# Kernel tuning notes

Measured on AMD Instinct MI355X. Metric: run time of the kernel, lower is better.

The kernel has to match this reference:

```python
import jax, jax.numpy as jnp
import numpy as np


def setup_inputs() -> dict:
    key = jax.random.key(0)
    ks = jax.random.split(key, 5)
    B, C, H, W = 8, 256, 64, 64
    Cr = 32  # in_channels // reduction_ratio
    s_in = 1.0 / np.sqrt(C)
    x = jax.random.normal(ks[0], (B, C, H, W), dtype=jnp.float32)
    Wq = jax.random.normal(ks[1], (Cr, C), dtype=jnp.float32) * s_in
    Wk = jax.random.normal(ks[2], (Cr, C), dtype=jnp.float32) * s_in
    Wv = jax.random.normal(ks[3], (C, C), dtype=jnp.float32) * s_in
    bq = jnp.zeros((Cr,), dtype=jnp.float32)
    bk = jnp.zeros((Cr,), dtype=jnp.float32)
    bv = jnp.zeros((C,), dtype=jnp.float32)
    gamma = jnp.ones((1,), dtype=jnp.float32)
    return {"x": x, "Wq": Wq, "bq": bq, "Wk": Wk, "bk": bk, "Wv": Wv, "bv": bv, "gamma": gamma}


def reference(x, Wq, bq, Wk, bk, Wv, bv, gamma):
    B, C, H, W = x.shape
    N = H * W
    xf = x.reshape(B, C, N)  # 1x1 conv == per-pixel linear over channels
    q = jnp.einsum('oc,bcn->bon', Wq, xf) + bq[None, :, None]   # [B, Cr, N]
    k = jnp.einsum('oc,bcn->bon', Wk, xf) + bk[None, :, None]   # [B, Cr, N]
    v = jnp.einsum('oc,bcn->bon', Wv, xf) + bv[None, :, None]   # [B, C, N]
    # correlations[b, i, j] = sum_c q[b, c, i] * k[b, c, j]
    corr = jnp.einsum('bci,bcj->bij', q, k)                     # [B, N, N]
    # NOTE: softmax over dim=1 (the i / query axis), as in the original torch code
    beta = jax.nn.softmax(corr, axis=1)
    att = gamma[0] * jnp.einsum('bci,bij->bcj', v, beta)        # [B, C, N]
    return att.reshape(B, C, H, W) + x
```

## Files before the change

### kernel.cpp

```cpp
#include <hip/hip_runtime.h>
#include <hip/hip_bf16.h>

typedef short bf16x8 __attribute__((ext_vector_type(8)));
typedef float f32x4 __attribute__((ext_vector_type(4)));
typedef unsigned short u16;

#define LOG2E 1.44269504088896340736f

__device__ __forceinline__ u16 f2bf(float f) {
    unsigned u = __float_as_uint(f);
    u += 0x7fffu + ((u >> 16) & 1u);
    return (u16)(u >> 16);
}
__device__ __forceinline__ float bf2f(u16 h) {
    return __uint_as_float(((unsigned)h) << 16);
}

__global__ void k_prep(const float* __restrict__ Wq, const float* __restrict__ bq,
                       const float* __restrict__ Wk, const float* __restrict__ bk,
                       const float* __restrict__ Wv, const float* __restrict__ bv,
                       u16* __restrict__ Whi, u16* __restrict__ Wlo,
                       float* __restrict__ bias) {
    int idx = blockIdx.x * 256 + threadIdx.x;
    if (idx >= 320 * 256) return;
    int row = idx >> 8, c = idx & 255;
    float w, b;
    if (row < 256)      { w = Wv[row * 256 + c];                  b = bv[row]; }
    else if (row < 288) { w = Wq[(row - 256) * 256 + c] * LOG2E;  b = bq[row - 256] * LOG2E; }
    else                { w = Wk[(row - 288) * 256 + c];          b = bk[row - 288]; }
    u16 hi = f2bf(w);
    Whi[idx] = hi;
    Wlo[idx] = f2bf(w - bf2f(hi));
    if (c == 0) bias[row] = b;
}

#define XPAD 264

__global__ __launch_bounds__(256) void k_proj(
    const float* __restrict__ x, const u16* __restrict__ Whi,
    const u16* __restrict__ Wlo, const float* __restrict__ bias,
    u16* __restrict__ qt, u16* __restrict__ kt, u16* __restrict__ vbf) {
    __shared__ __attribute__((aligned(16))) u16 xh[64 * XPAD];
    __shared__ __attribute__((aligned(16))) u16 xl[64 * XPAD];
    int bid = blockIdx.x;
    int b = bid & 7, nt = bid >> 3;
    int n0 = nt * 64;
    int t = threadIdx.x;
    int lane = t & 63, w = t >> 6;
    int lr = lane & 15, lk = lane >> 4;

    {
        int n = t & 63;
        int cg = t >> 6;
        for (int it = 0; it < 8; ++it) {
            int c8 = (it * 4 + cg) * 8;
            bf16x8 hv, lv;
#pragma unroll
            for (int u = 0; u < 8; ++u) {
                float xv = x[((size_t)(b * 256 + c8 + u)) * 4096 + n0 + n];
                u16 hu = f2bf(xv);
                hv[u] = (short)hu;
                lv[u] = (short)f2bf(xv - bf2f(hu));
            }
            *(bf16x8*)&xh[n * XPAD + c8] = hv;
            *(bf16x8*)&xl[n * XPAD + c8] = lv;
        }
    }
    __syncthreads();

    f32x4 acc[5][4];
#pragma unroll
    for (int i = 0; i < 5; i++)
#pragma unroll
        for (int j = 0; j < 4; j++) acc[i][j] = (f32x4){0.f, 0.f, 0.f, 0.f};

    for (int cs = 0; cs < 8; ++cs) {
        int c0 = cs * 32;
        bf16x8 ah[5], al[5], bh[4], bl[4];
#pragma unroll
        for (int mt = 0; mt < 5; ++mt) {
            int row = (w * 5 + mt) * 16 + lr;
            ah[mt] = *(const bf16x8*)&Whi[row * 256 + c0 + lk * 8];
            al[mt] = *(const bf16x8*)&Wlo[row * 256 + c0 + lk * 8];
        }
#pragma unroll
        for (int ns = 0; ns < 4; ++ns) {
            int np = ns * 16 + lr;
            bh[ns] = *(const bf16x8*)&xh[np * XPAD + c0 + lk * 8];
            bl[ns] = *(const bf16x8*)&xl[np * XPAD + c0 + lk * 8];
        }
#pragma unroll
        for (int mt = 0; mt < 5; ++mt)
#pragma unroll
            for (int ns = 0; ns < 4; ++ns) {
                acc[mt][ns] = __builtin_amdgcn_mfma_f32_16x16x32_bf16(ah[mt], bh[ns], acc[mt][ns], 0, 0, 0);
                acc[mt][ns] = __builtin_amdgcn_mfma_f32_16x16x32_bf16(ah[mt], bl[ns], acc[mt][ns], 0, 0, 0);
                acc[mt][ns] = __builtin_amdgcn_mfma_f32_16x16x32_bf16(al[mt], bh[ns], acc[mt][ns], 0, 0, 0);
            }
    }

#pragma unroll
    for (int mt = 0; mt < 5; ++mt) {
        int tile = w * 5 + mt;
#pragma unroll
        for (int ns = 0; ns < 4; ++ns) {
#pragma unroll
            for (int r = 0; r < 4; ++r) {
                int row = tile * 16 + lk * 4 + r;
                int n = n0 + ns * 16 + lr;
                float val = acc[mt][ns][r] + bias[row];
                if (row < 256) {
                    vbf[((size_t)(b * 256 + row)) * 4096 + n] = f2bf(val);
                } else if (row < 288) {
                    u16 hi = f2bf(val);
                    size_t base = ((size_t)(b * 4096 + n)) * 64 + (row - 256);
                    qt[base] = hi;
                    qt[base + 32] = f2bf(val - bf2f(hi));
                } else {
                    u16 hi = f2bf(val);
                    size_t base = ((size_t)(b * 4096 + n)) * 64 + (row - 288);
                    kt[base] = hi;
                    kt[base + 32] = f2bf(val - bf2f(hi));
                }
            }
        }
    }
}

#define PSTR 72

__global__ __launch_bounds__(256, 2) void k_attn(
    const u16* __restrict__ qt, const u16* __restrict__ kt,
    const u16* __restrict__ vbf, const float* __restrict__ x,
    const float* __restrict__ gamma, float* __restrict__ out) {
    __shared__ __attribute__((aligned(16))) u16 P[2][4][16][PSTR];
    __shared__ float sc[2][64];
    __shared__ float lbuf[64];
    int bid = blockIdx.x;
    int b = bid & 7, jt = bid >> 3;
    int t = threadIdx.x;
    int lane = t & 63, w = t >> 6;
    int lr = lane & 15, lk = lane >> 4;
    int j0 = jt * 64;
    int jw = j0 + w * 16;

    size_t kb = ((size_t)(b * 4096 + jw + lr)) * 64 + lk * 8;
    bf16x8 khi = *(const bf16x8*)&kt[kb];
    bf16x8 klo = *(const bf16x8*)&kt[kb + 32];

    f32x4 acc[4][4];
#pragma unroll
    for (int i = 0; i < 4; i++)
#pragma unroll
        for (int j = 0; j < 4; j++) acc[i][j] = (f32x4){0.f, 0.f, 0.f, 0.f};
    float mcur = -3.0e38f, lsum = 0.f;
    const f32x4 zero = {0.f, 0.f, 0.f, 0.f};

    for (int it = 0; it < 64; ++it) {
        int i0 = it * 64;
        int p = it & 1;

        bf16x8 qh[4], ql[4];
#pragma unroll
        for (int g = 0; g < 4; ++g) {
            size_t qb = ((size_t)(b * 4096 + i0 + g * 16 + lr)) * 64 + lk * 8;
            qh[g] = *(const bf16x8*)&qt[qb];
            ql[g] = *(const bf16x8*)&qt[qb + 32];
        }
        bf16x8 av[2][4];
#pragma unroll
        for (int ks = 0; ks < 2; ++ks)
#pragma unroll
            for (int ct = 0; ct < 4; ++ct)
                av[ks][ct] = *(const bf16x8*)&vbf[((size_t)(b * 256 + w * 64 + ct * 16 + lr)) * 4096
                                                  + i0 + ks * 32 + lk * 8];

        f32x4 s[4];
#pragma unroll
        for (int g = 0; g < 4; ++g) {
            s[g] = __builtin_amdgcn_mfma_f32_16x16x32_bf16(qh[g], khi, zero, 0, 0, 0);
            s[g] = __builtin_amdgcn_mfma_f32_16x16x32_bf16(qh[g], klo, s[g], 0, 0, 0);
            s[g] = __builtin_amdgcn_mfma_f32_16x16x32_bf16(ql[g], khi, s[g], 0, 0, 0);
        }

        float tm = -3.0e38f;
#pragma unroll
        for (int g = 0; g < 4; ++g)
            tm = fmaxf(tm, fmaxf(fmaxf(s[g][0], s[g][1]), fmaxf(s[g][2], s[g][3])));
        tm = fmaxf(tm, __shfl_xor(tm, 16));
        tm = fmaxf(tm, __shfl_xor(tm, 32));
        float mnew = fmaxf(mcur, tm);
        float scale = exp2f(mcur - mnew);
        mcur = mnew;
        lsum *= scale;
#pragma unroll
        for (int g = 0; g < 4; ++g) {
            float p0 = exp2f(s[g][0] - mcur), p1 = exp2f(s[g][1] - mcur);
            float p2 = exp2f(s[g][2] - mcur), p3 = exp2f(s[g][3] - mcur);
            lsum += (p0 + p1) + (p2 + p3);
            uint2 pk;
            pk.x = ((unsigned)f2bf(p1) << 16) | f2bf(p0);
            pk.y = ((unsigned)f2bf(p3) << 16) | f2bf(p2);
            *(uint2*)&P[p][w][lr][g * 16 + lk * 4] = pk;
        }
        if (lk == 0) sc[p][w * 16 + lr] = scale;
        __syncthreads();

        float rs[4];
#pragma unroll
        for (int js = 0; js < 4; ++js) rs[js] = sc[p][js * 16 + lr];
        if (__any((rs[0] != 1.f) | (rs[1] != 1.f) | (rs[2] != 1.f) | (rs[3] != 1.f))) {
#pragma unroll
            for (int ct = 0; ct < 4; ++ct)
#pragma unroll
                for (int js = 0; js < 4; ++js)
#pragma unroll
                    for (int r = 0; r < 4; ++r) acc[ct][js][r] *= rs[js];
        }
#pragma unroll
        for (int ks = 0; ks < 2; ++ks) {
            bf16x8 bp[4];
#pragma unroll
            for (int js = 0; js < 4; ++js)
                bp[js] = *(const bf16x8*)&P[p][js][lr][ks * 32 + lk * 8];
#pragma unroll
            for (int ct = 0; ct < 4; ++ct)
#pragma unroll
                for (int js = 0; js < 4; ++js)
                    acc[ct][js] = __builtin_amdgcn_mfma_f32_16x16x32_bf16(av[ks][ct], bp[js], acc[ct][js], 0, 0, 0);
        }
    }

    lsum += __shfl_xor(lsum, 16);
    lsum += __shfl_xor(lsum, 32);
    __syncthreads();
    if (lk == 0) lbuf[w * 16 + lr] = lsum;
    __syncthreads();
    float g = gamma[0];
    float linv[4];
#pragma unroll
    for (int js = 0; js < 4; ++js) linv[js] = g / lbuf[js * 16 + lr];
#pragma unroll
    for (int ct = 0; ct < 4; ++ct)
#pragma unroll
        for (int r = 0; r < 4; ++r) {
            int c = w * 64 + ct * 16 + lk * 4 + r;
            size_t base = ((size_t)(b * 256 + c)) * 4096 + j0;
#pragma unroll
            for (int js = 0; js < 4; ++js) {
                int j = js * 16 + lr;
                out[base + j] = acc[ct][js][r] * linv[js] + x[base + j];
            }
        }
}

extern "C" void kernel_launch(void* const* d_in, const int* in_sizes, int n_in,
                              void* d_out, int out_size, void* d_ws, size_t ws_size,
                              hipStream_t stream) {
    const float* x = (const float*)d_in[0];
    const float* Wq = (const float*)d_in[1];
    const float* bq = (const float*)d_in[2];
    const float* Wk = (const float*)d_in[3];
    const float* bk = (const float*)d_in[4];
    const float* Wv = (const float*)d_in[5];
    const float* bv = (const float*)d_in[6];
    const float* gamma = (const float*)d_in[7];

    char* ws = (char*)d_ws;
    u16* Whi = (u16*)ws;
    u16* Wlo = (u16*)(ws + 163840);
    float* bias = (float*)(ws + 327680);
    u16* qt = (u16*)(ws + 329216);
    u16* kt = (u16*)(ws + 329216 + 4194304);
    u16* vbf = (u16*)(ws + 329216 + 8388608);

    k_prep<<<320, 256, 0, stream>>>(Wq, bq, Wk, bk, Wv, bv, Whi, Wlo, bias);
    k_proj<<<512, 256, 0, stream>>>(x, Whi, Wlo, bias, qt, kt, vbf);
    k_attn<<<512, 256, 0, stream>>>(qt, kt, vbf, x, gamma, (float*)d_out);
}
```

Before: 356.3 us.

## Split attention block into producer and consumer waves for softmax/PV overlap

Each block now has 8 waves instead of 4. Four producer waves compute QK scores and the online-softmax tile for the next step into the double-buffered LDS P and scale arrays. Four consumer waves load V and run the PV MFMAs on the current tile, with one barrier per iteration. The aim is to overlap the exp and softmax work with the matrix accumulation and to spread V-load latency across more waves. The cost is doubled thread count per block, idle producers at the epilogue, and different occupancy and register limits from the new launch bounds.

```diff
diff --git a/kernel.cpp b/kernel.cpp
--- a/kernel.cpp
+++ b/kernel.cpp
@@ -129,7 +129,7 @@
 
 #define PSTR 72
 
-__global__ __launch_bounds__(256, 2) void k_attn(
+__global__ __launch_bounds__(512, 4) void k_attn(
     const u16* __restrict__ qt, const u16* __restrict__ kt,
     const u16* __restrict__ vbf, const float* __restrict__ x,
     const float* __restrict__ gamma, float* __restrict__ out) {
@@ -142,24 +142,23 @@
     int lane = t & 63, w = t >> 6;
     int lr = lane & 15, lk = lane >> 4;
     int j0 = jt * 64;
-    int jw = j0 + w * 16;
-
-    size_t kb = ((size_t)(b * 4096 + jw + lr)) * 64 + lk * 8;
+    int wp = w & 3;
+    bool is_prod = (w < 4);
+
+    size_t kb = ((size_t)(b * 4096 + j0 + wp * 16 + lr)) * 64 + lk * 8;
     bf16x8 khi = *(const bf16x8*)&kt[kb];
     bf16x8 klo = *(const bf16x8*)&kt[kb + 32];
 
+    float mcur = -3.0e38f, lsum = 0.f;
     f32x4 acc[4][4];
 #pragma unroll
     for (int i = 0; i < 4; i++)
 #pragma unroll
         for (int j = 0; j < 4; j++) acc[i][j] = (f32x4){0.f, 0.f, 0.f, 0.f};
-    float mcur = -3.0e38f, lsum = 0.f;
     const f32x4 zero = {0.f, 0.f, 0.f, 0.f};
 
-    for (int it = 0; it < 64; ++it) {
-        int i0 = it * 64;
-        int p = it & 1;
-
+    auto prod_step = [&](int it) {
+        int i0 = it * 64, p = it & 1;
         bf16x8 qh[4], ql[4];
 #pragma unroll
         for (int g = 0; g < 4; ++g) {
@@ -167,14 +166,6 @@
             qh[g] = *(const bf16x8*)&qt[qb];
             ql[g] = *(const bf16x8*)&qt[qb + 32];
         }
-        bf16x8 av[2][4];
-#pragma unroll
-        for (int ks = 0; ks < 2; ++ks)
-#pragma unroll
-            for (int ct = 0; ct < 4; ++ct)
-                av[ks][ct] = *(const bf16x8*)&vbf[((size_t)(b * 256 + w * 64 + ct * 16 + lr)) * 4096
-                                                  + i0 + ks * 32 + lk * 8];
-
         f32x4 s[4];
 #pragma unroll
         for (int g = 0; g < 4; ++g) {
@@ -182,7 +173,6 @@
             s[g] = __builtin_amdgcn_mfma_f32_16x16x32_bf16(qh[g], klo, s[g], 0, 0, 0);
             s[g] = __builtin_amdgcn_mfma_f32_16x16x32_bf16(ql[g], khi, s[g], 0, 0, 0);
         }
-
         float tm = -3.0e38f;
 #pragma unroll
         for (int g = 0; g < 4; ++g)
@@ -201,11 +191,18 @@
             uint2 pk;
             pk.x = ((unsigned)f2bf(p1) << 16) | f2bf(p0);
             pk.y = ((unsigned)f2bf(p3) << 16) | f2bf(p2);
-            *(uint2*)&P[p][w][lr][g * 16 + lk * 4] = pk;
-        }
-        if (lk == 0) sc[p][w * 16 + lr] = scale;
-        __syncthreads();
-
+            *(uint2*)&P[p][wp][lr][g * 16 + lk * 4] = pk;
+        }
+        if (lk == 0) sc[p][wp * 16 + lr] = scale;
+    };
+
+    auto cons_step = [&](int it) {
+        int i0 = it * 64, p = it & 1;
+        bf16x8 av0[4];
+#pragma unroll
+        for (int ct = 0; ct < 4; ++ct)
+            av0[ct] = *(const bf16x8*)&vbf[((size_t)(b * 256 + wp * 64 + ct * 16 + lr)) * 4096
+                                           + i0 + lk * 8];
         float rs[4];
 #pragma unroll
         for (int js = 0; js < 4; ++js) rs[js] = sc[p][js * 16 + lr];
@@ -217,41 +214,69 @@
 #pragma unroll
                     for (int r = 0; r < 4; ++r) acc[ct][js][r] *= rs[js];
         }
-#pragma unroll
-        for (int ks = 0; ks < 2; ++ks) {
+        bf16x8 av1[4];
+#pragma unroll
+        for (int ct = 0; ct < 4; ++ct)
+            av1[ct] = *(const bf16x8*)&vbf[((size_t)(b * 256 + wp * 64 + ct * 16 + lr)) * 4096
+                                           + i0 + 32 + lk * 8];
+        {
             bf16x8 bp[4];
 #pragma unroll
             for (int js = 0; js < 4; ++js)
-                bp[js] = *(const bf16x8*)&P[p][js][lr][ks * 32 + lk * 8];
+                bp[js] = *(const bf16x8*)&P[p][js][lr][lk * 8];
 #pragma unroll
             for (int ct = 0; ct < 4; ++ct)
 #pragma unroll
                 for (int js = 0; js < 4; ++js)
-                    acc[ct][js] = __builtin_amdgcn_mfma_f32_16x16x32_bf16(av[ks][ct], bp[js], acc[ct][js], 0, 0, 0);
-        }
-    }
-
-    lsum += __shfl_xor(lsum, 16);
-    lsum += __shfl_xor(lsum, 32);
+                    acc[ct][js] = __builtin_amdgcn_mfma_f32_16x16x32_bf16(av0[ct], bp[js], acc[ct][js], 0, 0, 0);
+        }
+        {
+            bf16x8 bp[4];
+#pragma unroll
+            for (int js = 0; js < 4; ++js)
+                bp[js] = *(const bf16x8*)&P[p][js][lr][32 + lk * 8];
+#pragma unroll
+            for (int ct = 0; ct < 4; ++ct)
+#pragma unroll
+                for (int js = 0; js < 4; ++js)
+                    acc[ct][js] = __builtin_amdgcn_mfma_f32_16x16x32_bf16(av1[ct], bp[js], acc[ct][js], 0, 0, 0);
+        }
+    };
+
+    if (is_prod) prod_step(0);
+    for (int tt = 0; tt < 64; ++tt) {
+        __syncthreads();
+        if (is_prod) {
+            if (tt < 63) prod_step(tt + 1);
+        } else {
+            cons_step(tt);
+        }
+    }
+
+    if (is_prod) {
+        lsum += __shfl_xor(lsum, 16);
+        lsum += __shfl_xor(lsum, 32);
+        if (lk == 0) lbuf[wp * 16 + lr] = lsum;
+    }
     __syncthreads();
-    if (lk == 0) lbuf[w * 16 + lr] = lsum;
-    __syncthreads();
-    float g = gamma[0];
-    float linv[4];
-#pragma unroll
-    for (int js = 0; js < 4; ++js) linv[js] = g / lbuf[js * 16 + lr];
-#pragma unroll
-    for (int ct = 0; ct < 4; ++ct)
-#pragma unroll
-        for (int r = 0; r < 4; ++r) {
-            int c = w * 64 + ct * 16 + lk * 4 + r;
-            size_t base = ((size_t)(b * 256 + c)) * 4096 + j0;
-#pragma unroll
-            for (int js = 0; js < 4; ++js) {
-                int j = js * 16 + lr;
-                out[base + j] = acc[ct][js][r] * linv[js] + x[base + j];
+    if (!is_prod) {
+        float g = gamma[0];
+        float linv[4];
+#pragma unroll
+        for (int js = 0; js < 4; ++js) linv[js] = g / lbuf[js * 16 + lr];
+#pragma unroll
+        for (int ct = 0; ct < 4; ++ct)
+#pragma unroll
+            for (int r = 0; r < 4; ++r) {
+                int c = wp * 64 + ct * 16 + lk * 4 + r;
+                size_t base = ((size_t)(b * 256 + c)) * 4096 + j0;
+#pragma unroll
+                for (int js = 0; js < 4; ++js) {
+                    int j = js * 16 + lr;
+                    out[base + j] = acc[ct][js][r] * linv[js] + x[base + j];
+                }
             }
-        }
+    }
 }
 
 extern "C" void kernel_launch(void* const* d_in, const int* in_sizes, int n_in,
@@ -276,5 +301,5 @@
 
     k_prep<<<320, 256, 0, stream>>>(Wq, bq, Wk, bk, Wv, bv, Whi, Wlo, bias);
     k_proj<<<512, 256, 0, stream>>>(x, Whi, Wlo, bias, qt, kt, vbf);
-    k_attn<<<512, 256, 0, stream>>>(qt, kt, vbf, x, gamma, (float*)d_out);
-}
+    k_attn<<<512, 512, 0, stream>>>(qt, kt, vbf, x, gamma, (float*)d_out);
+}
```

Result: slower. 402.9 us (+13.1%).

## Split softmax into max/sum prepass and rescale-free attention pass with prefetch

Applied to the files above, without the earlier changes.

Adds a separate kernel that computes the per-column softmax max and normalizer over all queries, so the main attention kernel can use the exact final max and skip the online rescaling of accumulators and the shared scale exchange. The attention loop is also restructured to double-buffer Q fragment loads, prefetching the next tile before the PV MFMAs, and it loads V after the softmax step. The cost is recomputing the QK^T scores twice (three MFMAs per tile in both passes) plus an extra launch and small global buffers.

```diff
diff --git a/kernel.cpp b/kernel.cpp
--- a/kernel.cpp
+++ b/kernel.cpp
@@ -127,39 +127,24 @@
     }
 }
 
-#define PSTR 72
-
-__global__ __launch_bounds__(256, 2) void k_attn(
+__global__ __launch_bounds__(256, 2) void k_ml(
     const u16* __restrict__ qt, const u16* __restrict__ kt,
-    const u16* __restrict__ vbf, const float* __restrict__ x,
-    const float* __restrict__ gamma, float* __restrict__ out) {
-    __shared__ __attribute__((aligned(16))) u16 P[2][4][16][PSTR];
-    __shared__ float sc[2][64];
-    __shared__ float lbuf[64];
+    float* __restrict__ Mg, float* __restrict__ Lg) {
     int bid = blockIdx.x;
     int b = bid & 7, jt = bid >> 3;
     int t = threadIdx.x;
     int lane = t & 63, w = t >> 6;
     int lr = lane & 15, lk = lane >> 4;
-    int j0 = jt * 64;
-    int jw = j0 + w * 16;
+    int jw = jt * 64 + w * 16;
 
     size_t kb = ((size_t)(b * 4096 + jw + lr)) * 64 + lk * 8;
     bf16x8 khi = *(const bf16x8*)&kt[kb];
     bf16x8 klo = *(const bf16x8*)&kt[kb + 32];
-
-    f32x4 acc[4][4];
-#pragma unroll
-    for (int i = 0; i < 4; i++)
-#pragma unroll
-        for (int j = 0; j < 4; j++) acc[i][j] = (f32x4){0.f, 0.f, 0.f, 0.f};
-    float mcur = -3.0e38f, lsum = 0.f;
     const f32x4 zero = {0.f, 0.f, 0.f, 0.f};
 
+    float m = -3.0e38f, sum = 0.f;
     for (int it = 0; it < 64; ++it) {
         int i0 = it * 64;
-        int p = it & 1;
-
         bf16x8 qh[4], ql[4];
 #pragma unroll
         for (int g = 0; g < 4; ++g) {
@@ -167,14 +152,6 @@
             qh[g] = *(const bf16x8*)&qt[qb];
             ql[g] = *(const bf16x8*)&qt[qb + 32];
         }
-        bf16x8 av[2][4];
-#pragma unroll
-        for (int ks = 0; ks < 2; ++ks)
-#pragma unroll
-            for (int ct = 0; ct < 4; ++ct)
-                av[ks][ct] = *(const bf16x8*)&vbf[((size_t)(b * 256 + w * 64 + ct * 16 + lr)) * 4096
-                                                  + i0 + ks * 32 + lk * 8];
-
         f32x4 s[4];
 #pragma unroll
         for (int g = 0; g < 4; ++g) {
@@ -182,40 +159,92 @@
             s[g] = __builtin_amdgcn_mfma_f32_16x16x32_bf16(qh[g], klo, s[g], 0, 0, 0);
             s[g] = __builtin_amdgcn_mfma_f32_16x16x32_bf16(ql[g], khi, s[g], 0, 0, 0);
         }
-
         float tm = -3.0e38f;
 #pragma unroll
         for (int g = 0; g < 4; ++g)
             tm = fmaxf(tm, fmaxf(fmaxf(s[g][0], s[g][1]), fmaxf(s[g][2], s[g][3])));
-        tm = fmaxf(tm, __shfl_xor(tm, 16));
-        tm = fmaxf(tm, __shfl_xor(tm, 32));
-        float mnew = fmaxf(mcur, tm);
-        float scale = exp2f(mcur - mnew);
-        mcur = mnew;
-        lsum *= scale;
-#pragma unroll
-        for (int g = 0; g < 4; ++g) {
-            float p0 = exp2f(s[g][0] - mcur), p1 = exp2f(s[g][1] - mcur);
-            float p2 = exp2f(s[g][2] - mcur), p3 = exp2f(s[g][3] - mcur);
-            lsum += (p0 + p1) + (p2 + p3);
+        float mnew = fmaxf(m, tm);
+        sum *= exp2f(m - mnew);
+        m = mnew;
+#pragma unroll
+        for (int g = 0; g < 4; ++g) {
+            sum += exp2f(s[g][0] - m) + exp2f(s[g][1] - m)
+                 + exp2f(s[g][2] - m) + exp2f(s[g][3] - m);
+        }
+    }
+#pragma unroll
+    for (int d = 16; d <= 32; d <<= 1) {
+        float pm = __shfl_xor(m, d), ps = __shfl_xor(sum, d);
+        float m2 = fmaxf(m, pm);
+        sum = sum * exp2f(m - m2) + ps * exp2f(pm - m2);
+        m = m2;
+    }
+    if (lane < 16) {
+        Mg[b * 4096 + jw + lr] = m;
+        Lg[b * 4096 + jw + lr] = sum;
+    }
+}
+
+#define PSTR 72
+
+__global__ __launch_bounds__(256, 2) void k_attn(
+    const u16* __restrict__ qt, const u16* __restrict__ kt,
+    const u16* __restrict__ vbf, const float* __restrict__ Mg,
+    const float* __restrict__ Lg, const float* __restrict__ x,
+    const float* __restrict__ gamma, float* __restrict__ out) {
+    __shared__ __attribute__((aligned(16))) u16 P[2][4][16][PSTR];
+    int bid = blockIdx.x;
+    int b = bid & 7, jt = bid >> 3;
+    int t = threadIdx.x;
+    int lane = t & 63, w = t >> 6;
+    int lr = lane & 15, lk = lane >> 4;
+    int j0 = jt * 64, jw = j0 + w * 16;
+
+    size_t kb = ((size_t)(b * 4096 + jw + lr)) * 64 + lk * 8;
+    bf16x8 khi = *(const bf16x8*)&kt[kb];
+    bf16x8 klo = *(const bf16x8*)&kt[kb + 32];
+    float mcol = Mg[b * 4096 + jw + lr];
+
+    f32x4 acc[4][4];
+#pragma unroll
+    for (int i = 0; i < 4; i++)
+#pragma unroll
+        for (int j = 0; j < 4; j++) acc[i][j] = (f32x4){0.f, 0.f, 0.f, 0.f};
+    const f32x4 zero = {0.f, 0.f, 0.f, 0.f};
+
+    auto step = [&](int p, int itc, bf16x8 (&qh)[4], bf16x8 (&ql)[4],
+                    bf16x8 (&qhn)[4], bf16x8 (&qln)[4]) {
+        int i0 = itc * 64;
+        f32x4 s[4];
+#pragma unroll
+        for (int g = 0; g < 4; ++g) {
+            s[g] = __builtin_amdgcn_mfma_f32_16x16x32_bf16(qh[g], khi, zero, 0, 0, 0);
+            s[g] = __builtin_amdgcn_mfma_f32_16x16x32_bf16(qh[g], klo, s[g], 0, 0, 0);
+            s[g] = __builtin_amdgcn_mfma_f32_16x16x32_bf16(ql[g], khi, s[g], 0, 0, 0);
+        }
+#pragma unroll
+        for (int g = 0; g < 4; ++g) {
+            float p0 = exp2f(s[g][0] - mcol), p1 = exp2f(s[g][1] - mcol);
+            float p2 = exp2f(s[g][2] - mcol), p3 = exp2f(s[g][3] - mcol);
             uint2 pk;
             pk.x = ((unsigned)f2bf(p1) << 16) | f2bf(p0);
             pk.y = ((unsigned)f2bf(p3) << 16) | f2bf(p2);
             *(uint2*)&P[p][w][lr][g * 16 + lk * 4] = pk;
         }
-        if (lk == 0) sc[p][w * 16 + lr] = scale;
+        bf16x8 av[8];
+#pragma unroll
+        for (int ks = 0; ks < 2; ++ks)
+#pragma unroll
+            for (int ct = 0; ct < 4; ++ct)
+                av[ks * 4 + ct] = *(const bf16x8*)&vbf[((size_t)(b * 256 + w * 64 + ct * 16 + lr)) * 4096
+                                                       + i0 + ks * 32 + lk * 8];
         __syncthreads();
-
-        float rs[4];
-#pragma unroll
-        for (int js = 0; js < 4; ++js) rs[js] = sc[p][js * 16 + lr];
-        if (__any((rs[0] != 1.f) | (rs[1] != 1.f) | (rs[2] != 1.f) | (rs[3] != 1.f))) {
-#pragma unroll
-            for (int ct = 0; ct < 4; ++ct)
-#pragma unroll
-                for (int js = 0; js < 4; ++js)
-#pragma unroll
-                    for (int r = 0; r < 4; ++r) acc[ct][js][r] *= rs[js];
+        int i0n = ((itc + 1) & 63) * 64;
+#pragma unroll
+        for (int g = 0; g < 4; ++g) {
+            size_t qb = ((size_t)(b * 4096 + i0n + g * 16 + lr)) * 64 + lk * 8;
+            qhn[g] = *(const bf16x8*)&qt[qb];
+            qln[g] = *(const bf16x8*)&qt[qb + 32];
         }
 #pragma unroll
         for (int ks = 0; ks < 2; ++ks) {
@@ -227,19 +256,26 @@
             for (int ct = 0; ct < 4; ++ct)
 #pragma unroll
                 for (int js = 0; js < 4; ++js)
-                    acc[ct][js] = __builtin_amdgcn_mfma_f32_16x16x32_bf16(av[ks][ct], bp[js], acc[ct][js], 0, 0, 0);
-        }
-    }
-
-    lsum += __shfl_xor(lsum, 16);
-    lsum += __shfl_xor(lsum, 32);
-    __syncthreads();
-    if (lk == 0) lbuf[w * 16 + lr] = lsum;
-    __syncthreads();
+                    acc[ct][js] = __builtin_amdgcn_mfma_f32_16x16x32_bf16(av[ks * 4 + ct], bp[js], acc[ct][js], 0, 0, 0);
+        }
+    };
+
+    bf16x8 qhA[4], qlA[4], qhB[4], qlB[4];
+#pragma unroll
+    for (int g = 0; g < 4; ++g) {
+        size_t qb = ((size_t)(b * 4096 + g * 16 + lr)) * 64 + lk * 8;
+        qhA[g] = *(const bf16x8*)&qt[qb];
+        qlA[g] = *(const bf16x8*)&qt[qb + 32];
+    }
+    for (int it = 0; it < 64; it += 2) {
+        step(0, it,     qhA, qlA, qhB, qlB);
+        step(1, it + 1, qhB, qlB, qhA, qlA);
+    }
+
     float g = gamma[0];
     float linv[4];
 #pragma unroll
-    for (int js = 0; js < 4; ++js) linv[js] = g / lbuf[js * 16 + lr];
+    for (int js = 0; js < 4; ++js) linv[js] = g / Lg[b * 4096 + j0 + js * 16 + lr];
 #pragma unroll
     for (int ct = 0; ct < 4; ++ct)
 #pragma unroll
@@ -273,8 +309,11 @@
     u16* qt = (u16*)(ws + 329216);
     u16* kt = (u16*)(ws + 329216 + 4194304);
     u16* vbf = (u16*)(ws + 329216 + 8388608);
+    float* Mg = (float*)(ws + 329216 + 25165824);
+    float* Lg = (float*)(ws + 329216 + 25165824 + 131072);
 
     k_prep<<<320, 256, 0, stream>>>(Wq, bq, Wk, bk, Wv, bv, Whi, Wlo, bias);
     k_proj<<<512, 256, 0, stream>>>(x, Whi, Wlo, bias, qt, kt, vbf);
-    k_attn<<<512, 256, 0, stream>>>(qt, kt, vbf, x, gamma, (float*)d_out);
-}
+    k_ml<<<512, 256, 0, stream>>>(qt, kt, Mg, Lg);
+    k_attn<<<512, 256, 0, stream>>>(qt, kt, vbf, Mg, Lg, x, gamma, (float*)d_out);
+}
```

Measured after the change: 490.0 us. 1.38x slower.

## Replace online softmax max with precomputed norm bound and retile attention

Applied to the files above, without the earlier changes.

Adds a small kernel that computes a per-batch upper bound on the logits from the maximum q and k norms (Cauchy-Schwarz), minus a margin. The attention kernel uses this fixed shift instead of a running max, which removes the per-tile max reduction, the scale broadcast through shared memory and the accumulator rescaling. The attention kernel is also retiled to 32-column tiles with 1024 blocks and a higher occupancy target, and q fragments are prefetched one iteration ahead. The fixed shift risks underflow or division by zero if a column's true logits sit far below the bound, and the bound kernel runs on only 8 blocks.

```diff
diff --git a/kernel.cpp b/kernel.cpp
--- a/kernel.cpp
+++ b/kernel.cpp
@@ -127,119 +127,145 @@
     }
 }
 
+__global__ __launch_bounds__(256) void k_bound(
+    const u16* __restrict__ qt, const u16* __restrict__ kt,
+    float* __restrict__ Sh) {
+    __shared__ float rq[4], rk[4];
+    int b = blockIdx.x;
+    int t = threadIdx.x;
+    int lane = t & 63, w = t >> 6;
+    float qm = 0.f, km = 0.f;
+    for (int n = t; n < 4096; n += 256) {
+        size_t base = ((size_t)(b * 4096 + n)) * 64;
+        float sq = 0.f, sk = 0.f;
+#pragma unroll
+        for (int g = 0; g < 4; ++g) {
+            bf16x8 vq = *(const bf16x8*)&qt[base + g * 8];
+            bf16x8 vk = *(const bf16x8*)&kt[base + g * 8];
+#pragma unroll
+            for (int u = 0; u < 8; ++u) {
+                float a = bf2f((u16)vq[u]), c = bf2f((u16)vk[u]);
+                sq += a * a;
+                sk += c * c;
+            }
+        }
+        qm = fmaxf(qm, sq);
+        km = fmaxf(km, sk);
+    }
+#pragma unroll
+    for (int d = 1; d < 64; d <<= 1) {
+        qm = fmaxf(qm, __shfl_xor(qm, d));
+        km = fmaxf(km, __shfl_xor(km, d));
+    }
+    if (lane == 0) { rq[w] = qm; rk[w] = km; }
+    __syncthreads();
+    if (t == 0) {
+        float a = fmaxf(fmaxf(rq[0], rq[1]), fmaxf(rq[2], rq[3]));
+        float c = fmaxf(fmaxf(rk[0], rk[1]), fmaxf(rk[2], rk[3]));
+        Sh[b] = fmaxf(0.f, sqrtf(a) * sqrtf(c) - 80.f);
+    }
+}
+
 #define PSTR 72
 
-__global__ __launch_bounds__(256, 2) void k_attn(
+__global__ __launch_bounds__(256, 4) void k_attn(
     const u16* __restrict__ qt, const u16* __restrict__ kt,
-    const u16* __restrict__ vbf, const float* __restrict__ x,
-    const float* __restrict__ gamma, float* __restrict__ out) {
-    __shared__ __attribute__((aligned(16))) u16 P[2][4][16][PSTR];
-    __shared__ float sc[2][64];
-    __shared__ float lbuf[64];
+    const u16* __restrict__ vbf, const float* __restrict__ Sh,
+    const float* __restrict__ x, const float* __restrict__ gamma,
+    float* __restrict__ out) {
+    __shared__ __attribute__((aligned(16))) u16 P[2][2][16][PSTR];
+    __shared__ float Ls[4][16];
     int bid = blockIdx.x;
     int b = bid & 7, jt = bid >> 3;
     int t = threadIdx.x;
     int lane = t & 63, w = t >> 6;
     int lr = lane & 15, lk = lane >> 4;
-    int j0 = jt * 64;
-    int jw = j0 + w * 16;
-
-    size_t kb = ((size_t)(b * 4096 + jw + lr)) * 64 + lk * 8;
+    int j0 = jt * 32;
+    int js = w & 1, ih = w >> 1;
+
+    size_t kb = ((size_t)(b * 4096 + j0 + js * 16 + lr)) * 64 + lk * 8;
     bf16x8 khi = *(const bf16x8*)&kt[kb];
     bf16x8 klo = *(const bf16x8*)&kt[kb + 32];
-
-    f32x4 acc[4][4];
+    float shift = Sh[b];
+
+    f32x4 acc[4][2];
 #pragma unroll
     for (int i = 0; i < 4; i++)
 #pragma unroll
-        for (int j = 0; j < 4; j++) acc[i][j] = (f32x4){0.f, 0.f, 0.f, 0.f};
-    float mcur = -3.0e38f, lsum = 0.f;
+        for (int j = 0; j < 2; j++) acc[i][j] = (f32x4){0.f, 0.f, 0.f, 0.f};
+    float lsum = 0.f;
     const f32x4 zero = {0.f, 0.f, 0.f, 0.f};
 
-    for (int it = 0; it < 64; ++it) {
-        int i0 = it * 64;
-        int p = it & 1;
-
-        bf16x8 qh[4], ql[4];
-#pragma unroll
-        for (int g = 0; g < 4; ++g) {
-            size_t qb = ((size_t)(b * 4096 + i0 + g * 16 + lr)) * 64 + lk * 8;
-            qh[g] = *(const bf16x8*)&qt[qb];
-            ql[g] = *(const bf16x8*)&qt[qb + 32];
-        }
-        bf16x8 av[2][4];
-#pragma unroll
-        for (int ks = 0; ks < 2; ++ks)
-#pragma unroll
-            for (int ct = 0; ct < 4; ++ct)
-                av[ks][ct] = *(const bf16x8*)&vbf[((size_t)(b * 256 + w * 64 + ct * 16 + lr)) * 4096
-                                                  + i0 + ks * 32 + lk * 8];
-
-        f32x4 s[4];
-#pragma unroll
-        for (int g = 0; g < 4; ++g) {
+    auto step = [&](int p, int itc, bf16x8 (&qh)[2], bf16x8 (&ql)[2],
+                    bf16x8 (&qhn)[2], bf16x8 (&qln)[2]) {
+        int i0 = itc * 64;
+        f32x4 s[2];
+#pragma unroll
+        for (int g = 0; g < 2; ++g) {
             s[g] = __builtin_amdgcn_mfma_f32_16x16x32_bf16(qh[g], khi, zero, 0, 0, 0);
             s[g] = __builtin_amdgcn_mfma_f32_16x16x32_bf16(qh[g], klo, s[g], 0, 0, 0);
             s[g] = __builtin_amdgcn_mfma_f32_16x16x32_bf16(ql[g], khi, s[g], 0, 0, 0);
         }
-
-        float tm = -3.0e38f;
-#pragma unroll
-        for (int g = 0; g < 4; ++g)
-            tm = fmaxf(tm, fmaxf(fmaxf(s[g][0], s[g][1]), fmaxf(s[g][2], s[g][3])));
-        tm = fmaxf(tm, __shfl_xor(tm, 16));
-        tm = fmaxf(tm, __shfl_xor(tm, 32));
-        float mnew = fmaxf(mcur, tm);
-        float scale = exp2f(mcur - mnew);
-        mcur = mnew;
-        lsum *= scale;
-#pragma unroll
-        for (int g = 0; g < 4; ++g) {
-            float p0 = exp2f(s[g][0] - mcur), p1 = exp2f(s[g][1] - mcur);
-            float p2 = exp2f(s[g][2] - mcur), p3 = exp2f(s[g][3] - mcur);
+#pragma unroll
+        for (int g = 0; g < 2; ++g) {
+            float p0 = exp2f(s[g][0] - shift), p1 = exp2f(s[g][1] - shift);
+            float p2 = exp2f(s[g][2] - shift), p3 = exp2f(s[g][3] - shift);
             lsum += (p0 + p1) + (p2 + p3);
             uint2 pk;
             pk.x = ((unsigned)f2bf(p1) << 16) | f2bf(p0);
             pk.y = ((unsigned)f2bf(p3) << 16) | f2bf(p2);
-            *(uint2*)&P[p][w][lr][g * 16 + lk * 4] = pk;
-        }
-        if (lk == 0) sc[p][w * 16 + lr] = scale;
+            *(uint2*)&P[p][js][lr][ih * 32 + g * 16 + lk * 4] = pk;
+        }
+        bf16x8 av[8];
+#pragma unroll
+        for (int ks = 0; ks < 2; ++ks)
+#pragma unroll
+            for (int ct = 0; ct < 4; ++ct)
+                av[ks * 4 + ct] = *(const bf16x8*)&vbf[((size_t)(b * 256 + w * 64 + ct * 16 + lr)) * 4096
+                                                       + i0 + ks * 32 + lk * 8];
         __syncthreads();
-
-        float rs[4];
-#pragma unroll
-        for (int js = 0; js < 4; ++js) rs[js] = sc[p][js * 16 + lr];
-        if (__any((rs[0] != 1.f) | (rs[1] != 1.f) | (rs[2] != 1.f) | (rs[3] != 1.f))) {
+        int i0n = ((itc + 1) & 63) * 64;
+#pragma unroll
+        for (int g = 0; g < 2; ++g) {
+            size_t qb = ((size_t)(b * 4096 + i0n + ih * 32 + g * 16 + lr)) * 64 + lk * 8;
+            qhn[g] = *(const bf16x8*)&qt[qb];
+            qln[g] = *(const bf16x8*)&qt[qb + 32];
+        }
+#pragma unroll
+        for (int ks = 0; ks < 2; ++ks) {
+            bf16x8 bp[2];
+#pragma unroll
+            for (int j2 = 0; j2 < 2; ++j2)
+                bp[j2] = *(const bf16x8*)&P[p][j2][lr][ks * 32 + lk * 8];
 #pragma unroll
             for (int ct = 0; ct < 4; ++ct)
 #pragma unroll
-                for (int js = 0; js < 4; ++js)
-#pragma unroll
-                    for (int r = 0; r < 4; ++r) acc[ct][js][r] *= rs[js];
-        }
-#pragma unroll
-        for (int ks = 0; ks < 2; ++ks) {
-            bf16x8 bp[4];
-#pragma unroll
-            for (int js = 0; js < 4; ++js)
-                bp[js] = *(const bf16x8*)&P[p][js][lr][ks * 32 + lk * 8];
-#pragma unroll
-            for (int ct = 0; ct < 4; ++ct)
-#pragma unroll
-                for (int js = 0; js < 4; ++js)
-                    acc[ct][js] = __builtin_amdgcn_mfma_f32_16x16x32_bf16(av[ks][ct], bp[js], acc[ct][js], 0, 0, 0);
-        }
+                for (int j2 = 0; j2 < 2; ++j2)
+                    acc[ct][j2] = __builtin_amdgcn_mfma_f32_16x16x32_bf16(av[ks * 4 + ct], bp[j2], acc[ct][j2], 0, 0, 0);
+        }
+    };
+
+    bf16x8 qhA[2], qlA[2], qhB[2], qlB[2];
+#pragma unroll
+    for (int g = 0; g < 2; ++g) {
+        size_t qb = ((size_t)(b * 4096 + ih * 32 + g * 16 + lr)) * 64 + lk * 8;
+        qhA[g] = *(const bf16x8*)&qt[qb];
+        qlA[g] = *(const bf16x8*)&qt[qb + 32];
+    }
+    for (int it = 0; it < 64; it += 2) {
+        step(0, it,     qhA, qlA, qhB, qlB);
+        step(1, it + 1, qhB, qlB, qhA, qlA);
     }
 
     lsum += __shfl_xor(lsum, 16);
     lsum += __shfl_xor(lsum, 32);
-    __syncthreads();
-    if (lk == 0) lbuf[w * 16 + lr] = lsum;
+    if (lane < 16) Ls[w][lr] = lsum;
     __syncthreads();
     float g = gamma[0];
-    float linv[4];
-#pragma unroll
-    for (int js = 0; js < 4; ++js) linv[js] = g / lbuf[js * 16 + lr];
+    float linv[2];
+#pragma unroll
+    for (int j2 = 0; j2 < 2; ++j2)
+        linv[j2] = g / (Ls[j2][lr] + Ls[j2 + 2][lr]);
 #pragma unroll
     for (int ct = 0; ct < 4; ++ct)
 #pragma unroll
@@ -247,9 +273,9 @@
             int c = w * 64 + ct * 16 + lk * 4 + r;
             size_t base = ((size_t)(b * 256 + c)) * 4096 + j0;
 #pragma unroll
-            for (int js = 0; js < 4; ++js) {
-                int j = js * 16 + lr;
-                out[base + j] = acc[ct][js][r] * linv[js] + x[base + j];
+            for (int j2 = 0; j2 < 2; ++j2) {
+                int j = j2 * 16 + lr;
+                out[base + j] = acc[ct][j2][r] * linv[j2] + x[base + j];
             }
         }
 }
@@ -273,8 +299,10 @@
     u16* qt = (u16*)(ws + 329216);
     u16* kt = (u16*)(ws + 329216 + 4194304);
     u16* vbf = (u16*)(ws + 329216 + 8388608);
+    float* Shf = (float*)(ws + 329216 + 25165824);
 
     k_prep<<<320, 256, 0, stream>>>(Wq, bq, Wk, bk, Wv, bv, Whi, Wlo, bias);
     k_proj<<<512, 256, 0, stream>>>(x, Whi, Wlo, bias, qt, kt, vbf);
-    k_attn<<<512, 256, 0, stream>>>(qt, kt, vbf, x, gamma, (float*)d_out);
-}
+    k_bound<<<8, 256, 0, stream>>>(qt, kt, Shf);
+    k_attn<<<1024, 256, 0, stream>>>(qt, kt, vbf, Shf, x, gamma, (float*)d_out);
+}
```

New measurement: 493.0 us. 1.38x slower.
